# Performance work log

Hardware: AMD Instinct MI355X
Metric: run time of the kernel (lower is better)

Reference implementation:

```python
import jax, jax.numpy as jnp
import numpy as np


def _maxpool2d(x, k):
    # Non-overlapping max pool, kernel=stride=k, over NCHW spatial dims.
    return jax.lax.reduce_window(
        x, -jnp.inf, jax.lax.max,
        window_dimensions=(1, 1, k, k),
        window_strides=(1, 1, k, k),
        padding='VALID')


def setup_inputs() -> dict:
    key = jax.random.key(0)
    k1, k2, k3, k4, k5 = jax.random.split(key, 5)
    B = 8
    return {
        'in1': jax.random.normal(k1, (B, 256, 64, 64), jnp.float32),
        'in2': jax.random.normal(k2, (B, 128, 128, 128), jnp.float32),
        'in3': jax.random.normal(k3, (B, 64, 256, 256), jnp.float32),
        'in4': jax.random.normal(k4, (B, 32, 512, 512), jnp.float32),
        'pure_ff': jax.random.normal(k5, (B, 512, 32, 32), jnp.float32),
    }


def reference(in1, in2, in3, in4, pure_ff):
    # The original concatenates n identical copies along channels and then
    # max-pools. Max pooling is per-channel, so this is algebraically
    # identical to pooling once and tiling channels afterward (much cheaper).
    x1 = jnp.tile(_maxpool2d(in1, 2), (1, 2, 1, 1))    # [B, 512, 32, 32]
    x2 = jnp.tile(_maxpool2d(in2, 4), (1, 4, 1, 1))    # [B, 512, 32, 32]
    x3 = jnp.tile(_maxpool2d(in3, 8), (1, 8, 1, 1))    # [B, 512, 32, 32]
    x4 = jnp.tile(_maxpool2d(in4, 16), (1, 16, 1, 1))  # [B, 512, 32, 32]
    return jax.nn.relu(x1 + x2 + x3 + x4 + pure_ff)
```

## Files before the change

kernel.cpp:

```cpp
#include <hip/hip_runtime.h>
#include <math.h>


#define P1_OFF 0
#define P2_OFF 2097152
#define P3_OFF 3145728
#define P4_OFF 3670016

__device__ __forceinline__ float max4(float4 v) {
    return fmaxf(fmaxf(v.x, v.y), fmaxf(v.z, v.w));
}

template <int K>
__device__ __forceinline__ float pool_window(const float* __restrict__ p, int W) {
    float m = -INFINITY;
#pragma unroll
    for (int r = 0; r < K; ++r) {
        const float* row = p + r * W;
        if (K == 2) {
            float2 v = *(const float2*)row;
            m = fmaxf(m, fmaxf(v.x, v.y));
        } else {
#pragma unroll
            for (int c = 0; c < K; c += 4) {
                float4 v = *(const float4*)(row + c);
                m = fmaxf(m, max4(v));
            }
        }
    }
    return m;
}

__global__ __launch_bounds__(256) void pool_all_kernel(
    const float* __restrict__ in1, const float* __restrict__ in2,
    const float* __restrict__ in3, const float* __restrict__ in4,
    float* __restrict__ ws) {
    const int blk = blockIdx.x;
    const int tid = threadIdx.x;

    if (blk < 1024) {
        const int opix = blk * 256 + tid;
        const int ow = opix & 31, oh = (opix >> 5) & 31, bc = opix >> 10;
        const float* p = in4 + bc * (512 * 512) + (oh * 16) * 512 + ow * 16;
        ws[P4_OFF + opix] = pool_window<16>(p, 512);
    } else if (blk < 3072) {
        const int opix = (blk - 1024) * 256 + tid;
        const int ow = opix & 31, oh = (opix >> 5) & 31, bc = opix >> 10;
        const float* p = in3 + bc * (256 * 256) + (oh * 8) * 256 + ow * 8;
        ws[P3_OFF + opix] = pool_window<8>(p, 256);
    } else if (blk < 7168) {
        const int opix = (blk - 3072) * 256 + tid;
        const int ow = opix & 31, oh = (opix >> 5) & 31, bc = opix >> 10;
        const float* p = in2 + bc * (128 * 128) + (oh * 4) * 128 + ow * 4;
        ws[P2_OFF + opix] = pool_window<4>(p, 128);
    } else {
        const int opix = (blk - 7168) * 256 + tid;
        const int ow = opix & 31, oh = (opix >> 5) & 31, bc = opix >> 10;
        const float* p = in1 + bc * (64 * 64) + (oh * 2) * 64 + ow * 2;
        ws[P1_OFF + opix] = pool_window<2>(p, 64);
    }
}

__global__ __launch_bounds__(256) void combine_kernel(
    const float* __restrict__ ff, const float* __restrict__ ws,
    float* __restrict__ out) {
    const int t = blockIdx.x * 256 + threadIdx.x;
    const int b = t >> 17;
    const int r = t & 131071;
    const int c = r >> 8;
    const int q = r & 255;

    const float4* ff4 = (const float4*)ff;
    const float4* p1 = (const float4*)(ws + P1_OFF);
    const float4* p2 = (const float4*)(ws + P2_OFF);
    const float4* p3 = (const float4*)(ws + P3_OFF);
    const float4* p4 = (const float4*)(ws + P4_OFF);

    float4 a  = ff4[t];
    float4 v1 = p1[(b * 256 + (c & 255)) * 256 + q];
    float4 v2 = p2[(b * 128 + (c & 127)) * 256 + q];
    float4 v3 = p3[(b *  64 + (c &  63)) * 256 + q];
    float4 v4 = p4[(b *  32 + (c &  31)) * 256 + q];

    float4 o;
    o.x = fmaxf(a.x + v1.x + v2.x + v3.x + v4.x, 0.0f);
    o.y = fmaxf(a.y + v1.y + v2.y + v3.y + v4.y, 0.0f);
    o.z = fmaxf(a.z + v1.z + v2.z + v3.z + v4.z, 0.0f);
    o.w = fmaxf(a.w + v1.w + v2.w + v3.w + v4.w, 0.0f);
    ((float4*)out)[t] = o;
}

extern "C" void kernel_launch(void* const* d_in, const int* in_sizes, int n_in,
                              void* d_out, int out_size, void* d_ws, size_t ws_size,
                              hipStream_t stream) {
    const float* in1 = (const float*)d_in[0];
    const float* in2 = (const float*)d_in[1];
    const float* in3 = (const float*)d_in[2];
    const float* in4 = (const float*)d_in[3];
    const float* ff  = (const float*)d_in[4];
    float* ws  = (float*)d_ws;
    float* out = (float*)d_out;

    pool_all_kernel<<<15360, 256, 0, stream>>>(in1, in2, in3, in4, ws);
    combine_kernel<<<4096, 256, 0, stream>>>(ff, ws, out);
}
```

Before: 500.5 us.

## Fuse pooling and combine into one kernel using shared memory

Merges the four max-pool passes and the add+ReLU combine into a single kernel. Each block pools one spatial slice for all tiled source channels into shared memory, then writes the summed output for 16 output channels. This drops the workspace write/read round trip and the second launch. The cost is far fewer blocks (1024 instead of 15360) with more serial load work per thread, which may reduce memory-level parallelism on a bandwidth-bound read of roughly 1 GB of input.

```diff
diff --git a/kernel.cpp b/kernel.cpp
--- a/kernel.cpp
+++ b/kernel.cpp
@@ -1,93 +1,100 @@
 #include <hip/hip_runtime.h>
 #include <math.h>
 
-
-#define P1_OFF 0
-#define P2_OFF 2097152
-#define P3_OFF 3145728
-#define P4_OFF 3670016
 
 __device__ __forceinline__ float max4(float4 v) {
     return fmaxf(fmaxf(v.x, v.y), fmaxf(v.z, v.w));
 }
 
-template <int K>
-__device__ __forceinline__ float pool_window(const float* __restrict__ p, int W) {
-    float m = -INFINITY;
-#pragma unroll
-    for (int r = 0; r < K; ++r) {
-        const float* row = p + r * W;
-        if (K == 2) {
-            float2 v = *(const float2*)row;
-            m = fmaxf(m, fmaxf(v.x, v.y));
-        } else {
-#pragma unroll
-            for (int c = 0; c < K; c += 4) {
-                float4 v = *(const float4*)(row + c);
-                m = fmaxf(m, max4(v));
-            }
-        }
-    }
-    return m;
-}
-
-__global__ __launch_bounds__(256) void pool_all_kernel(
+__global__ __launch_bounds__(256, 4) void fused_kernel(
     const float* __restrict__ in1, const float* __restrict__ in2,
     const float* __restrict__ in3, const float* __restrict__ in4,
-    float* __restrict__ ws) {
-    const int blk = blockIdx.x;
+    const float* __restrict__ ff, float* __restrict__ out) {
+
+    __shared__ float p4s[8][32];
+    __shared__ float p3s[2][8][32];
+    __shared__ float p2s[4][8][32];
+    __shared__ float p1s[8][8][32];
+
     const int tid = threadIdx.x;
+    const int bid = blockIdx.x;
+    const int s   = bid & 3;
+    const int m   = (bid >> 2) & 31;
+    const int b   = bid >> 7;
 
-    if (blk < 1024) {
-        const int opix = blk * 256 + tid;
-        const int ow = opix & 31, oh = (opix >> 5) & 31, bc = opix >> 10;
-        const float* p = in4 + bc * (512 * 512) + (oh * 16) * 512 + ow * 16;
-        ws[P4_OFF + opix] = pool_window<16>(p, 512);
-    } else if (blk < 3072) {
-        const int opix = (blk - 1024) * 256 + tid;
-        const int ow = opix & 31, oh = (opix >> 5) & 31, bc = opix >> 10;
-        const float* p = in3 + bc * (256 * 256) + (oh * 8) * 256 + ow * 8;
-        ws[P3_OFF + opix] = pool_window<8>(p, 256);
-    } else if (blk < 7168) {
-        const int opix = (blk - 3072) * 256 + tid;
-        const int ow = opix & 31, oh = (opix >> 5) & 31, bc = opix >> 10;
-        const float* p = in2 + bc * (128 * 128) + (oh * 4) * 128 + ow * 4;
-        ws[P2_OFF + opix] = pool_window<4>(p, 128);
-    } else {
-        const int opix = (blk - 7168) * 256 + tid;
-        const int ow = opix & 31, oh = (opix >> 5) & 31, bc = opix >> 10;
-        const float* p = in1 + bc * (64 * 64) + (oh * 2) * 64 + ow * 2;
-        ws[P1_OFF + opix] = pool_window<2>(p, 64);
+    const int col = tid & 31;
+    const int row = tid >> 5;
+    const int oh  = s * 8 + row;
+
+    {
+        const float* p = in4 + ((size_t)(b * 32 + m) * 512 + oh * 16) * 512
+                             + col * 16;
+        float mx = -INFINITY;
+#pragma unroll 4
+        for (int r = 0; r < 16; ++r) {
+#pragma unroll
+            for (int c = 0; c < 16; c += 4)
+                mx = fmaxf(mx, max4(*(const float4*)(p + r * 512 + c)));
+        }
+        p4s[row][col] = mx;
     }
-}
 
-__global__ __launch_bounds__(256) void combine_kernel(
-    const float* __restrict__ ff, const float* __restrict__ ws,
-    float* __restrict__ out) {
-    const int t = blockIdx.x * 256 + threadIdx.x;
-    const int b = t >> 17;
-    const int r = t & 131071;
-    const int c = r >> 8;
-    const int q = r & 255;
+#pragma unroll
+    for (int j = 0; j < 2; ++j) {
+        const float* p = in3 + ((size_t)(b * 64 + m + 32 * j) * 256 + oh * 8) * 256
+                             + col * 8;
+        float mx = -INFINITY;
+#pragma unroll
+        for (int r = 0; r < 8; ++r) {
+            mx = fmaxf(mx, max4(*(const float4*)(p + r * 256)));
+            mx = fmaxf(mx, max4(*(const float4*)(p + r * 256 + 4)));
+        }
+        p3s[j][row][col] = mx;
+    }
 
-    const float4* ff4 = (const float4*)ff;
-    const float4* p1 = (const float4*)(ws + P1_OFF);
-    const float4* p2 = (const float4*)(ws + P2_OFF);
-    const float4* p3 = (const float4*)(ws + P3_OFF);
-    const float4* p4 = (const float4*)(ws + P4_OFF);
+#pragma unroll
+    for (int j = 0; j < 4; ++j) {
+        const float* p = in2 + ((size_t)(b * 128 + m + 32 * j) * 128 + oh * 4) * 128
+                             + col * 4;
+        float mx = -INFINITY;
+#pragma unroll
+        for (int r = 0; r < 4; ++r)
+            mx = fmaxf(mx, max4(*(const float4*)(p + r * 128)));
+        p2s[j][row][col] = mx;
+    }
 
-    float4 a  = ff4[t];
-    float4 v1 = p1[(b * 256 + (c & 255)) * 256 + q];
-    float4 v2 = p2[(b * 128 + (c & 127)) * 256 + q];
-    float4 v3 = p3[(b *  64 + (c &  63)) * 256 + q];
-    float4 v4 = p4[(b *  32 + (c &  31)) * 256 + q];
+#pragma unroll
+    for (int j = 0; j < 8; ++j) {
+        const float* p = in1 + ((size_t)(b * 256 + m + 32 * j) * 64 + oh * 2) * 64
+                             + col * 2;
+        float2 v0 = *(const float2*)p;
+        float2 v1 = *(const float2*)(p + 64);
+        p1s[j][row][col] = fmaxf(fmaxf(v0.x, v0.y), fmaxf(v1.x, v1.y));
+    }
 
-    float4 o;
-    o.x = fmaxf(a.x + v1.x + v2.x + v3.x + v4.x, 0.0f);
-    o.y = fmaxf(a.y + v1.y + v2.y + v3.y + v4.y, 0.0f);
-    o.z = fmaxf(a.z + v1.z + v2.z + v3.z + v4.z, 0.0f);
-    o.w = fmaxf(a.w + v1.w + v2.w + v3.w + v4.w, 0.0f);
-    ((float4*)out)[t] = o;
+    __syncthreads();
+
+    const int ci  = tid >> 6;
+    const int idx = tid & 63;
+    const int r2  = idx >> 3;
+    const int q   = idx & 7;
+#pragma unroll
+    for (int pass = 0; pass < 4; ++pass) {
+        const int i = pass * 4 + ci;
+        const int c = m + 32 * i;
+        const size_t o4 = (size_t)(b * 512 + c) * 256 + (s * 8 + r2) * 8 + q;
+        float4 a  = ((const float4*)ff)[o4];
+        float4 v1 = *(const float4*)&p1s[i & 7][r2][q * 4];
+        float4 v2 = *(const float4*)&p2s[i & 3][r2][q * 4];
+        float4 v3 = *(const float4*)&p3s[i & 1][r2][q * 4];
+        float4 v4 = *(const float4*)&p4s[r2][q * 4];
+        float4 o;
+        o.x = fmaxf(a.x + v1.x + v2.x + v3.x + v4.x, 0.0f);
+        o.y = fmaxf(a.y + v1.y + v2.y + v3.y + v4.y, 0.0f);
+        o.z = fmaxf(a.z + v1.z + v2.z + v3.z + v4.z, 0.0f);
+        o.w = fmaxf(a.w + v1.w + v2.w + v3.w + v4.w, 0.0f);
+        ((float4*)out)[o4] = o;
+    }
 }
 
 extern "C" void kernel_launch(void* const* d_in, const int* in_sizes, int n_in,
@@ -98,9 +105,8 @@
     const float* in3 = (const float*)d_in[2];
     const float* in4 = (const float*)d_in[3];
     const float* ff  = (const float*)d_in[4];
-    float* ws  = (float*)d_ws;
     float* out = (float*)d_out;
+    (void)d_ws; (void)ws_size;
 
-    pool_all_kernel<<<15360, 256, 0, stream>>>(in1, in2, in3, in4, ws);
-    combine_kernel<<<4096, 256, 0, stream>>>(ff, ws, out);
+    fused_kernel<<<1024, 256, 0, stream>>>(in1, in2, in3, in4, ff, out);
 }
```

After: 497.4 us. About the same (-0.6%).
